# Performance work log

Measured on AMD Instinct MI355X. Metric: run time of the kernel, lower is better.

## Reference

```python
import jax, jax.numpy as jnp
import numpy as np
import math

D_MODEL = 1024
N_HEAD = 16
B, T = 4, 2048


def setup_inputs() -> dict:
    key = jax.random.key(0)
    ks = jax.random.split(key, 12)
    s = 1.0 / math.sqrt(D_MODEL)
    inp = {
        "q": jax.random.normal(ks[0], (B, T, D_MODEL), dtype=jnp.float32),
        "k": jax.random.normal(ks[1], (B, T, D_MODEL), dtype=jnp.float32),
        "v": jax.random.normal(ks[2], (B, T, D_MODEL), dtype=jnp.float32),
        "Wq": jax.random.uniform(ks[3], (D_MODEL, D_MODEL), jnp.float32, -s, s),
        "bq": jax.random.uniform(ks[4], (D_MODEL,), jnp.float32, -s, s),
        "Wk": jax.random.uniform(ks[5], (D_MODEL, D_MODEL), jnp.float32, -s, s),
        "bk": jax.random.uniform(ks[6], (D_MODEL,), jnp.float32, -s, s),
        "Wv": jax.random.uniform(ks[7], (D_MODEL, D_MODEL), jnp.float32, -s, s),
        "bv": jax.random.uniform(ks[8], (D_MODEL,), jnp.float32, -s, s),
        "Wo": jax.random.uniform(ks[9], (D_MODEL, D_MODEL), jnp.float32, -s, s),
        "bo": jax.random.uniform(ks[10], (D_MODEL,), jnp.float32, -s, s),
    }
    return inp


def reference(q, k, v, Wq, bq, Wk, bk, Wv, bv, Wo, bo):
    # NOTE: original module applies all three projections to `q` (k, v args unused)
    batch, time, dim = q.shape
    n_d = dim // N_HEAD
    # torch Linear: x @ W.T + b
    Q = (q @ Wq.T + bq).reshape(batch, time, N_HEAD, n_d).transpose(0, 2, 1, 3)
    K = (q @ Wk.T + bk).reshape(batch, time, N_HEAD, n_d).transpose(0, 2, 1, 3)
    V = (q @ Wv.T + bv).reshape(batch, time, N_HEAD, n_d).transpose(0, 2, 1, 3)
    # [B, H, T, T]
    score = jnp.einsum("bhqd,bhkd->bhqk", Q, K) / jnp.sqrt(jnp.float32(n_d))
    causal = jnp.tril(jnp.ones((time, time), dtype=bool))
    score = jnp.where(causal, score, -jnp.inf)
    # original uses Softmax(dim=-2): normalizes over the QUERY axis (faithful)
    attn = jax.nn.softmax(score, axis=-2)
    ctx = jnp.einsum("bhqk,bhkd->bhqd", attn, V)
    ctx = ctx.transpose(0, 2, 1, 3).reshape(batch, time, dim)
    return ctx @ Wo.T + bo
```

## Files before the change

### kernel.cpp

```cpp
#include <hip/hip_runtime.h>
#include <hip/hip_bf16.h>
#include <cstdint>
#include <cstddef>

typedef __bf16 bf16x8 __attribute__((ext_vector_type(8)));
typedef __bf16 bf16x4 __attribute__((ext_vector_type(4)));
typedef __bf16 bf16x2 __attribute__((ext_vector_type(2)));
typedef float  f32x4  __attribute__((ext_vector_type(4)));

static constexpr int TSEQ  = 2048;
static constexpr int DM    = 1024;
static constexpr int NH    = 16;
static constexpr int HD    = 64;
static constexpr int BATCH = 4;
static constexpr float SCL = 0.18033688011112042f;

__device__ __forceinline__ void gload16(const __bf16* g, __bf16* l) {
  __builtin_amdgcn_global_load_lds((const __attribute__((address_space(1))) void*)g,
                                   (__attribute__((address_space(3))) void*)l, 16, 0, 0);
}

#define PBAR()  asm volatile("s_barrier" ::: "memory")
#define LGKM()  asm volatile("s_waitcnt lgkmcnt(0)" ::: "memory")

__global__ __launch_bounds__(256) void cvt_kernel(const float* __restrict__ in,
                                                  __bf16* __restrict__ out, int n4) {
  int i = blockIdx.x * 256 + threadIdx.x;
  if (i < n4) {
    float4 v = reinterpret_cast<const float4*>(in)[i];
    bf16x4 o;
    o[0] = (__bf16)v.x; o[1] = (__bf16)v.y; o[2] = (__bf16)v.z; o[3] = (__bf16)v.w;
    reinterpret_cast<bf16x4*>(out)[i] = o;
  }
}

__global__ __launch_bounds__(256) void cvt4_kernel(
    const float* __restrict__ a, const float* __restrict__ bsrc,
    const float* __restrict__ c, const float* __restrict__ d,
    __bf16* __restrict__ oa, __bf16* __restrict__ ob,
    __bf16* __restrict__ oc, __bf16* __restrict__ od, int n4) {
  const float* src = (blockIdx.y == 0) ? a : (blockIdx.y == 1) ? bsrc
                    : (blockIdx.y == 2) ? c : d;
  __bf16* dst = (blockIdx.y == 0) ? oa : (blockIdx.y == 1) ? ob
               : (blockIdx.y == 2) ? oc : od;
  int i = blockIdx.x * 256 + threadIdx.x;
  if (i < n4) {
    float4 v = reinterpret_cast<const float4*>(src)[i];
    bf16x4 o;
    o[0] = (__bf16)v.x; o[1] = (__bf16)v.y; o[2] = (__bf16)v.z; o[3] = (__bf16)v.w;
    reinterpret_cast<bf16x4*>(dst)[i] = o;
  }
}

template <typename OUT_T>
__device__ __forceinline__ void gemm_body8(
    const __bf16* __restrict__ A, const __bf16* __restrict__ W,
    const float* __restrict__ bias, OUT_T* __restrict__ C,
    int i0, int o0, __bf16* lA, __bf16* lB) {
  const int tid = threadIdx.x;
  const int l = tid & 63, lr = l & 15, lg = l >> 4;
  const int w = tid >> 6;
  const int wr = w >> 2, wc = w & 3;

  f32x4 acc[8][4];
  const f32x4 fzero = {0.f, 0.f, 0.f, 0.f};
#pragma unroll
  for (int mi = 0; mi < 8; ++mi)
#pragma unroll
    for (int ni = 0; ni < 4; ++ni) acc[mi][ni] = fzero;

  const int s_row = tid >> 3;
  const int s_cc  = tid & 7;
  const __bf16* Ab = A + (size_t)i0 * DM;
  const __bf16* Wb = W + (size_t)o0 * DM;

  auto stage = [&](const __bf16* G, __bf16* L, int buf, int kt, int h) {
#pragma unroll
    for (int rr = 0; rr < 2; ++rr) {
      int row = h * 128 + rr * 64 + s_row;
      gload16(G + (size_t)row * DM + kt * 64 + ((s_cc ^ (row & 7)) << 3),
              L + buf * 16384 + (h * 128 + rr * 64) * 64 + tid * 8);
    }
  };
  auto rd = [&](const __bf16* base, int row, int ks) {
    int chunk = (ks * 4 + lg) ^ (row & 7);
    return *(const bf16x8*)(base + row * 64 + chunk * 8);
  };

  const int NT = DM / 64;

#pragma unroll
  for (int h = 0; h < 2; ++h) { stage(Ab, lA, 0, 0, h); stage(Wb, lB, 0, 0, h); }
#pragma unroll
  for (int h = 0; h < 2; ++h) { stage(Ab, lA, 1, 1, h); stage(Wb, lB, 1, 1, h); }
  asm volatile("s_waitcnt vmcnt(8)" ::: "memory");
  PBAR();

  for (int t = 0; t < NT; ++t) {
    const int cur = t & 1;
    const __bf16* cA = lA + cur * 16384;
    const __bf16* cB = lB + cur * 16384;
    const bool pre = (t + 2 < NT);

    bf16x8 afl[4][2], bfl[2][2], afh[4][2], bfh[2][2];

#pragma unroll
    for (int mi = 0; mi < 4; ++mi)
#pragma unroll
      for (int ks = 0; ks < 2; ++ks)
        afl[mi][ks] = rd(cA, wr * 64 + mi * 16 + lr, ks);
#pragma unroll
    for (int ni = 0; ni < 2; ++ni)
#pragma unroll
      for (int ks = 0; ks < 2; ++ks)
        bfl[ni][ks] = rd(cB, wc * 32 + ni * 16 + lr, ks);
    PBAR(); LGKM();
    __builtin_amdgcn_s_setprio(1);
#pragma unroll
    for (int mi = 0; mi < 4; ++mi)
#pragma unroll
      for (int ni = 0; ni < 2; ++ni)
#pragma unroll
        for (int ks = 0; ks < 2; ++ks)
          acc[mi][ni] = __builtin_amdgcn_mfma_f32_16x16x32_bf16(
              afl[mi][ks], bfl[ni][ks], acc[mi][ni], 0, 0, 0);
    __builtin_amdgcn_s_setprio(0);
    PBAR();

#pragma unroll
    for (int ni = 0; ni < 2; ++ni)
#pragma unroll
      for (int ks = 0; ks < 2; ++ks)
        bfh[ni][ks] = rd(cB, 128 + wc * 32 + ni * 16 + lr, ks);
    if (pre) stage(Wb, lB, cur, t + 2, 0);
    PBAR(); LGKM();
    __builtin_amdgcn_s_setprio(1);
#pragma unroll
    for (int mi = 0; mi < 4; ++mi)
#pragma unroll
      for (int ni = 0; ni < 2; ++ni)
#pragma unroll
        for (int ks = 0; ks < 2; ++ks)
          acc[mi][ni + 2] = __builtin_amdgcn_mfma_f32_16x16x32_bf16(
              afl[mi][ks], bfh[ni][ks], acc[mi][ni + 2], 0, 0, 0);
    __builtin_amdgcn_s_setprio(0);
    PBAR();

#pragma unroll
    for (int mi = 0; mi < 4; ++mi)
#pragma unroll
      for (int ks = 0; ks < 2; ++ks)
        afh[mi][ks] = rd(cA, 128 + wr * 64 + mi * 16 + lr, ks);
    if (pre) { stage(Ab, lA, cur, t + 2, 0); stage(Wb, lB, cur, t + 2, 1); }
    PBAR(); LGKM();
    __builtin_amdgcn_s_setprio(1);
#pragma unroll
    for (int mi = 0; mi < 4; ++mi)
#pragma unroll
      for (int ni = 0; ni < 2; ++ni)
#pragma unroll
        for (int ks = 0; ks < 2; ++ks)
          acc[mi + 4][ni] = __builtin_amdgcn_mfma_f32_16x16x32_bf16(
              afh[mi][ks], bfl[ni][ks], acc[mi + 4][ni], 0, 0, 0);
    __builtin_amdgcn_s_setprio(0);
    PBAR();

    if (pre) stage(Ab, lA, cur, t + 2, 1);
    if (pre)                asm volatile("s_waitcnt vmcnt(8)" ::: "memory");
    else if (t + 1 < NT)    asm volatile("s_waitcnt vmcnt(0)" ::: "memory");
    PBAR();
    __builtin_amdgcn_s_setprio(1);
#pragma unroll
    for (int mi = 0; mi < 4; ++mi)
#pragma unroll
      for (int ni = 0; ni < 2; ++ni)
#pragma unroll
        for (int ks = 0; ks < 2; ++ks)
          acc[mi + 4][ni + 2] = __builtin_amdgcn_mfma_f32_16x16x32_bf16(
              afh[mi][ks], bfh[ni][ks], acc[mi + 4][ni + 2], 0, 0, 0);
    __builtin_amdgcn_s_setprio(0);
    PBAR();
  }

#pragma unroll
  for (int ni = 0; ni < 4; ++ni) {
    int colb = (ni < 2) ? (wc * 32 + ni * 16) : (128 + wc * 32 + (ni - 2) * 16);
    int col = o0 + colb + lr;
    float bb = bias[col];
#pragma unroll
    for (int mi = 0; mi < 8; ++mi) {
      int rowb = (mi < 4) ? (wr * 64 + mi * 16) : (128 + wr * 64 + (mi - 4) * 16);
      int row = i0 + rowb + lg * 4;
#pragma unroll
      for (int r = 0; r < 4; ++r)
        C[(size_t)(row + r) * DM + col] = (OUT_T)(acc[mi][ni][r] + bb);
    }
  }
}

__global__ __launch_bounds__(512, 2) void gemm_qkv_kernel(
    const __bf16* __restrict__ A,
    const __bf16* __restrict__ W0, const __bf16* __restrict__ W1,
    const __bf16* __restrict__ W2,
    const float* __restrict__ b0, const float* __restrict__ b1,
    const float* __restrict__ b2,
    __bf16* __restrict__ O0, __bf16* __restrict__ O1, __bf16* __restrict__ O2) {
  __shared__ __align__(16) __bf16 lA[2 * 256 * 64];
  __shared__ __align__(16) __bf16 lB[2 * 256 * 64];
  const int flat = blockIdx.x;
  const int xcd = flat & 7, idx = flat >> 3;
  const int mi = xcd * 4 + idx / 12;
  const int nig = idx % 12;
  const int z = nig >> 2;
  const int o0 = (nig & 3) * 256;
  const __bf16* W = (z == 0) ? W0 : (z == 1) ? W1 : W2;
  const float* bias = (z == 0) ? b0 : (z == 1) ? b1 : b2;
  __bf16* C = (z == 0) ? O0 : (z == 1) ? O1 : O2;
  gemm_body8<__bf16>(A, W, bias, C, mi * 256, o0, lA, lB);
}

template <typename OUT_T>
__device__ __forceinline__ void gemm_body2(
    const __bf16* __restrict__ A, const __bf16* __restrict__ W,
    const float* __restrict__ bias, OUT_T* __restrict__ C,
    int i0, int o0, __bf16* lA, __bf16* lB) {
  const int tid = threadIdx.x;
  const int l = tid & 63, lr = l & 15, lg = l >> 4;
  const int w = tid >> 6;
  const int wr = w >> 2, wc = w & 3;

  f32x4 acc[4][4];
  const f32x4 fzero = {0.f, 0.f, 0.f, 0.f};
#pragma unroll
  for (int mi = 0; mi < 4; ++mi)
#pragma unroll
    for (int ni = 0; ni < 4; ++ni) acc[mi][ni] = fzero;

  const int s_row = tid >> 3;
  const int s_cc  = tid & 7;
  const int NT = DM / 64;

  {
#pragma unroll
    for (int n = 0; n < 2; ++n) {
      int row = n * 64 + s_row;
      gload16(A + (size_t)(i0 + row) * DM + ((s_cc ^ (row & 7)) << 3),
              lA + n * 4096 + tid * 8);
    }
#pragma unroll
    for (int n = 0; n < 4; ++n) {
      int row = n * 64 + s_row;
      gload16(W + (size_t)(o0 + row) * DM + ((s_cc ^ (row & 7)) << 3),
              lB + n * 4096 + tid * 8);
    }
  }
  asm volatile("s_waitcnt vmcnt(0)" ::: "memory");
  __syncthreads();

  for (int t = 0; t < NT; ++t) {
    const int cur = t & 1;
    if (t + 1 < NT) {
      const int k0 = (t + 1) * 64;
      const int nxt = cur ^ 1;
#pragma unroll
      for (int n = 0; n < 2; ++n) {
        int row = n * 64 + s_row;
        gload16(A + (size_t)(i0 + row) * DM + k0 + ((s_cc ^ (row & 7)) << 3),
                lA + nxt * 8192 + n * 4096 + tid * 8);
      }
#pragma unroll
      for (int n = 0; n < 4; ++n) {
        int row = n * 64 + s_row;
        gload16(W + (size_t)(o0 + row) * DM + k0 + ((s_cc ^ (row & 7)) << 3),
                lB + nxt * 16384 + n * 4096 + tid * 8);
      }
    }

    const __bf16* cA = lA + cur * 8192;
    const __bf16* cB = lB + cur * 16384;

    bf16x8 af[4][2], bf_[2][2];
#pragma unroll
    for (int mi = 0; mi < 4; ++mi)
#pragma unroll
      for (int ks = 0; ks < 2; ++ks) {
        int row = wr * 64 + mi * 16 + lr;
        int chunk = (ks * 4 + lg) ^ (row & 7);
        af[mi][ks] = *(const bf16x8*)(cA + row * 64 + chunk * 8);
      }
#pragma unroll
    for (int ni = 0; ni < 2; ++ni)
#pragma unroll
      for (int ks = 0; ks < 2; ++ks) {
        int row = wc * 64 + ni * 16 + lr;
        int chunk = (ks * 4 + lg) ^ (row & 7);
        bf_[ni][ks] = *(const bf16x8*)(cB + row * 64 + chunk * 8);
      }
    __builtin_amdgcn_s_setprio(1);
#pragma unroll
    for (int mi = 0; mi < 4; ++mi)
#pragma unroll
      for (int ni = 0; ni < 2; ++ni)
#pragma unroll
        for (int ks = 0; ks < 2; ++ks)
          acc[mi][ni] = __builtin_amdgcn_mfma_f32_16x16x32_bf16(
              af[mi][ks], bf_[ni][ks], acc[mi][ni], 0, 0, 0);
    __builtin_amdgcn_s_setprio(0);

#pragma unroll
    for (int ni = 0; ni < 2; ++ni)
#pragma unroll
      for (int ks = 0; ks < 2; ++ks) {
        int row = wc * 64 + (ni + 2) * 16 + lr;
        int chunk = (ks * 4 + lg) ^ (row & 7);
        bf_[ni][ks] = *(const bf16x8*)(cB + row * 64 + chunk * 8);
      }
    __builtin_amdgcn_s_setprio(1);
#pragma unroll
    for (int mi = 0; mi < 4; ++mi)
#pragma unroll
      for (int ni = 0; ni < 2; ++ni)
#pragma unroll
        for (int ks = 0; ks < 2; ++ks)
          acc[mi][ni + 2] = __builtin_amdgcn_mfma_f32_16x16x32_bf16(
              af[mi][ks], bf_[ni][ks], acc[mi][ni + 2], 0, 0, 0);
    __builtin_amdgcn_s_setprio(0);

    if (t + 1 < NT) {
      asm volatile("s_waitcnt vmcnt(0)" ::: "memory");
      __syncthreads();
    }
  }

#pragma unroll
  for (int ni = 0; ni < 4; ++ni) {
    int col = o0 + wc * 64 + ni * 16 + lr;
    float bb = bias[col];
#pragma unroll
    for (int mi = 0; mi < 4; ++mi) {
      int row = i0 + wr * 64 + mi * 16 + lg * 4;
#pragma unroll
      for (int r = 0; r < 4; ++r)
        C[(size_t)(row + r) * DM + col] = (OUT_T)(acc[mi][ni][r] + bb);
    }
  }
}

__global__ __launch_bounds__(512, 2) void gemm_out_kernel(
    const __bf16* __restrict__ A, const __bf16* __restrict__ W,
    const float* __restrict__ bias, float* __restrict__ C) {
  __shared__ __align__(16) __bf16 lA[2 * 128 * 64];
  __shared__ __align__(16) __bf16 lB[2 * 256 * 64];
  const int flat = blockIdx.x;
  const int xcd = flat & 7, idx = flat >> 3;
  const int mi = xcd * 8 + (idx & 7);
  const int ni = idx >> 3;
  gemm_body2<float>(A, W, bias, C, mi * 128, ni * 256, lA, lB);
}

__global__ __launch_bounds__(256) void colstats_kernel(
    const __bf16* __restrict__ Q, const __bf16* __restrict__ K,
    const __bf16* __restrict__ V, __bf16* __restrict__ VT) {
  const int flat = blockIdx.x;
  const int wid = (flat & 7) * 128 + (flat >> 3);
  const int g = wid >> 4, bx = wid & 15;
  const int h = g & 15, b = g >> 4;
  const int tid = threadIdx.x;
  const int w = tid >> 6, l = tid & 63, lr = l & 15, lg = l >> 4;
  const size_t base = (size_t)b * TSEQ * DM + (size_t)h * HD;

  __shared__ float part[4][64];
  __shared__ float invc[64];

  for (int ph = 0; ph < 2; ++ph) {
    const int kt = ph ? (31 - bx) : bx;
    const int k0 = kt * 64;

    bf16x8 kf[4][2];
#pragma unroll
    for (int ct = 0; ct < 4; ++ct)
#pragma unroll
      for (int ks = 0; ks < 2; ++ks)
        kf[ct][ks] = *(const bf16x8*)(K + base + (size_t)(k0 + ct * 16 + lr) * DM +
                                      ks * 32 + lg * 8);

    float csum[4] = {0.f, 0.f, 0.f, 0.f};
    const int nchunks = (TSEQ - k0) >> 4;
    for (int jj = w; jj < nchunks; jj += 4) {
      int qrow = k0 + jj * 16;
      bf16x8 a0 = *(const bf16x8*)(Q + base + (size_t)(qrow + lr) * DM + lg * 8);
      bf16x8 a1 = *(const bf16x8*)(Q + base + (size_t)(qrow + lr) * DM + 32 + lg * 8);
      const bool interior = (jj >= 4);
#pragma unroll
      for (int ct = 0; ct < 4; ++ct) {
        f32x4 s = {0.f, 0.f, 0.f, 0.f};
        s = __builtin_amdgcn_mfma_f32_16x16x32_bf16(a0, kf[ct][0], s, 0, 0, 0);
        s = __builtin_amdgcn_mfma_f32_16x16x32_bf16(a1, kf[ct][1], s, 0, 0, 0);
        if (interior) {
#pragma unroll
          for (int r = 0; r < 4; ++r) csum[ct] += __builtin_amdgcn_exp2f(s[r] * SCL);
        } else {
#pragma unroll
          for (int r = 0; r < 4; ++r) {
            int ql = jj * 16 + lg * 4 + r;
            int kl = ct * 16 + lr;
            float e = __builtin_amdgcn_exp2f(s[r] * SCL);
            csum[ct] += (ql >= kl) ? e : 0.f;
          }
        }
      }
    }

#pragma unroll
    for (int ct = 0; ct < 4; ++ct) {
      csum[ct] += __shfl_xor(csum[ct], 16, 64);
      csum[ct] += __shfl_xor(csum[ct], 32, 64);
    }

    if (l < 16) {
#pragma unroll
      for (int ct = 0; ct < 4; ++ct) part[w][ct * 16 + l] = csum[ct];
    }
    __syncthreads();
    if (tid < 64) {
      float c = part[0][tid] + part[1][tid] + part[2][tid] + part[3][tid];
      invc[tid] = 1.0f / c;
    }
    __syncthreads();

    const int d = tid >> 2, gq = tid & 3;
    size_t vtb = (((size_t)(b * NH + h)) * HD + d) * TSEQ + k0 + gq * 16;
#pragma unroll
    for (int kc = 0; kc < 16; kc += 2) {
      int kl = gq * 16 + kc;
      float v0 = (float)V[base + (size_t)(k0 + kl) * DM + d] * invc[kl];
      float v1 = (float)V[base + (size_t)(k0 + kl + 1) * DM + d] * invc[kl + 1];
      bf16x2 o; o[0] = (__bf16)v0; o[1] = (__bf16)v1;
      *(bf16x2*)(VT + vtb + kc) = o;
    }
    __syncthreads();
  }
}

__device__ __forceinline__ int swz(int e) { return e ^ (((e >> 6) & 7) << 3); }

__global__ __launch_bounds__(256, 4) void ctx_kernel(
    const __bf16* __restrict__ Q, const __bf16* __restrict__ K,
    const __bf16* __restrict__ VT, __bf16* __restrict__ CTX) {
  __shared__ __align__(16) __bf16 lK[4096];
  __shared__ __align__(16) __bf16 lV[4096];
  __shared__ __align__(16) __bf16 lP[8][16 * 88];
  const int flat = blockIdx.x;
  const int wid = (flat & 7) * 128 + (flat >> 3);
  const int g = wid >> 4, bx = wid & 15;
  const int h = g & 15, b = g >> 4;
  const int tid = threadIdx.x;
  const int w = tid >> 6, l = tid & 63, lr = l & 15, lg = l >> 4;
  const size_t base = (size_t)b * TSEQ * DM + (size_t)h * HD;
  const size_t vtb = ((size_t)(b * NH + h)) * HD * TSEQ;
  __bf16* pw1 = &lP[w][0];
  __bf16* pw2 = &lP[w + 4][0];

  const int qt1 = 31 - bx, qt2 = bx;
  const int q01 = qt1 * 64, q02 = qt2 * 64;

  const int srow = w * 8 + (l >> 3);
  const int scol = (((l & 7) ^ (l >> 3)) << 3);

  bf16x8 qf1[2], qf2[2];
#pragma unroll
  for (int ks = 0; ks < 2; ++ks) {
    qf1[ks] = *(const bf16x8*)(Q + base + (size_t)(q01 + w * 16 + lr) * DM + ks * 32 + lg * 8);
    qf2[ks] = *(const bf16x8*)(Q + base + (size_t)(q02 + w * 16 + lr) * DM + ks * 32 + lg * 8);
  }

  f32x4 acc1[4], acc2[4];
  const f32x4 fzero = {0.f, 0.f, 0.f, 0.f};
#pragma unroll
  for (int dt = 0; dt < 4; ++dt) { acc1[dt] = fzero; acc2[dt] = fzero; }

  for (int kt = 0; kt <= qt1; ++kt) {
    const int k0 = kt * 64;
    const bool two = (kt <= qt2);
    __syncthreads();
#pragma unroll
    for (int n = 0; n < 2; ++n) {
      gload16(K + base + (size_t)(k0 + n * 32 + srow) * DM + scol,
              lK + n * 2048 + w * 512);
      gload16(VT + vtb + (size_t)(n * 32 + srow) * TSEQ + k0 + scol,
              lV + n * 2048 + w * 512);
    }
    asm volatile("s_waitcnt vmcnt(0)" ::: "memory");
    __syncthreads();

    const bool diag1 = (kt == qt1), diag2 = (kt == qt2);
#pragma unroll
    for (int ct = 0; ct < 4; ++ct) {
      bf16x8 kb[2];
#pragma unroll
      for (int ks = 0; ks < 2; ++ks) {
        int e = (ct * 16 + lr) * 64 + ks * 32 + lg * 8;
        kb[ks] = *(const bf16x8*)(lK + swz(e));
      }
      {
        f32x4 s = {0.f, 0.f, 0.f, 0.f};
        s = __builtin_amdgcn_mfma_f32_16x16x32_bf16(kb[0], qf1[0], s, 0, 0, 0);
        s = __builtin_amdgcn_mfma_f32_16x16x32_bf16(kb[1], qf1[1], s, 0, 0, 0);
        bf16x4 pk;
        if (diag1) {
#pragma unroll
          for (int r = 0; r < 4; ++r) {
            int ql = w * 16 + lr, kl = ct * 16 + lg * 4 + r;
            pk[r] = (__bf16)((ql >= kl) ? __builtin_amdgcn_exp2f(s[r] * SCL) : 0.f);
          }
        } else {
#pragma unroll
          for (int r = 0; r < 4; ++r)
            pk[r] = (__bf16)__builtin_amdgcn_exp2f(s[r] * SCL);
        }
        *(bf16x4*)(pw1 + lr * 88 + ct * 16 + lg * 4) = pk;
      }
      if (two) {
        f32x4 s = {0.f, 0.f, 0.f, 0.f};
        s = __builtin_amdgcn_mfma_f32_16x16x32_bf16(kb[0], qf2[0], s, 0, 0, 0);
        s = __builtin_amdgcn_mfma_f32_16x16x32_bf16(kb[1], qf2[1], s, 0, 0, 0);
        bf16x4 pk;
        if (diag2) {
#pragma unroll
          for (int r = 0; r < 4; ++r) {
            int ql = w * 16 + lr, kl = ct * 16 + lg * 4 + r;
            pk[r] = (__bf16)((ql >= kl) ? __builtin_amdgcn_exp2f(s[r] * SCL) : 0.f);
          }
        } else {
#pragma unroll
          for (int r = 0; r < 4; ++r)
            pk[r] = (__bf16)__builtin_amdgcn_exp2f(s[r] * SCL);
        }
        *(bf16x4*)(pw2 + lr * 88 + ct * 16 + lg * 4) = pk;
      }
    }
    asm volatile("" ::: "memory");

    bf16x8 pa1[2], pa2[2];
#pragma unroll
    for (int ks = 0; ks < 2; ++ks)
      pa1[ks] = *(const bf16x8*)(pw1 + lr * 88 + ks * 32 + lg * 8);
    if (two) {
#pragma unroll
      for (int ks = 0; ks < 2; ++ks)
        pa2[ks] = *(const bf16x8*)(pw2 + lr * 88 + ks * 32 + lg * 8);
    }
#pragma unroll
    for (int dt = 0; dt < 4; ++dt) {
#pragma unroll
      for (int ks = 0; ks < 2; ++ks) {
        int e = (dt * 16 + lr) * 64 + ks * 32 + lg * 8;
        bf16x8 vb8 = *(const bf16x8*)(lV + swz(e));
        acc1[dt] = __builtin_amdgcn_mfma_f32_16x16x32_bf16(pa1[ks], vb8, acc1[dt], 0, 0, 0);
        if (two)
          acc2[dt] = __builtin_amdgcn_mfma_f32_16x16x32_bf16(pa2[ks], vb8, acc2[dt], 0, 0, 0);
      }
    }
  }

#pragma unroll
  for (int dt = 0; dt < 4; ++dt)
#pragma unroll
    for (int r = 0; r < 4; ++r) {
      CTX[base + (size_t)(q01 + w * 16 + lg * 4 + r) * DM + dt * 16 + lr] = (__bf16)acc1[dt][r];
      CTX[base + (size_t)(q02 + w * 16 + lg * 4 + r) * DM + dt * 16 + lr] = (__bf16)acc2[dt][r];
    }
}

extern "C" void kernel_launch(void* const* d_in, const int* in_sizes, int n_in,
                              void* d_out, int out_size, void* d_ws, size_t ws_size,
                              hipStream_t stream) {
  const float* q  = (const float*)d_in[0];
  const float* Wq = (const float*)d_in[3];
  const float* bq = (const float*)d_in[4];
  const float* Wk = (const float*)d_in[5];
  const float* bk = (const float*)d_in[6];
  const float* Wv = (const float*)d_in[7];
  const float* bv = (const float*)d_in[8];
  const float* Wo = (const float*)d_in[9];
  const float* bo = (const float*)d_in[10];
  float* out = (float*)d_out;

  const size_t NTOK = (size_t)BATCH * TSEQ;
  char* ws = (char*)d_ws;
  __bf16* qb  = (__bf16*)ws; ws += NTOK * DM * 2;
  __bf16* Wqb = (__bf16*)ws; ws += (size_t)DM * DM * 2;
  __bf16* Wkb = (__bf16*)ws; ws += (size_t)DM * DM * 2;
  __bf16* Wvb = (__bf16*)ws; ws += (size_t)DM * DM * 2;
  __bf16* Wob = (__bf16*)ws; ws += (size_t)DM * DM * 2;
  __bf16* Qp  = (__bf16*)ws; ws += NTOK * DM * 2;
  __bf16* Kp  = (__bf16*)ws; ws += NTOK * DM * 2;
  __bf16* Vp  = (__bf16*)ws; ws += NTOK * DM * 2;
  __bf16* VT  = (__bf16*)ws; ws += (size_t)BATCH * NH * HD * TSEQ * 2;
  __bf16* CTX = qb;

  const int nq4 = (int)(NTOK * DM / 4);
  const int nw4 = DM * DM / 4;
  cvt_kernel<<<(nq4 + 255) / 256, 256, 0, stream>>>(q, qb, nq4);
  cvt4_kernel<<<dim3((nw4 + 255) / 256, 4), 256, 0, stream>>>(
      Wq, Wk, Wv, Wo, Wqb, Wkb, Wvb, Wob, nw4);

  gemm_qkv_kernel<<<384, 512, 0, stream>>>(qb, Wqb, Wkb, Wvb, bq, bk, bv,
                                           Qp, Kp, Vp);

  colstats_kernel<<<1024, 256, 0, stream>>>(Qp, Kp, Vp, VT);
  ctx_kernel<<<1024, 256, 0, stream>>>(Qp, Kp, VT, CTX);

  gemm_out_kernel<<<256, 512, 0, stream>>>(CTX, Wob, bo, out);
}
```

Before: 208.7 us.

## Software-pipeline LDS fragment reads across GEMM phases and use contiguous warp tiles

The next tile's A-low and B-low fragments are now read from the other LDS buffer during the last MFMA phase of the current iteration. Partial lgkmcnt waits let the MFMAs start before every outstanding LDS read has returned. The warp-to-tile mapping changes from split halves (offset 128) to contiguous 128x64 per-warp blocks, and the epilogue indexing is updated to match. This is meant to hide LDS read latency behind matrix math. In exchange it keeps more fragment registers live across the loop and depends on correct ordering between the partial waits and the global-to-LDS staging.

Measured after the change: 234.3 us. 1.12x slower.

```diff
diff --git a/kernel.cpp b/kernel.cpp
--- a/kernel.cpp
+++ b/kernel.cpp
@@ -20,8 +20,8 @@
                                    (__attribute__((address_space(3))) void*)l, 16, 0, 0);
 }
 
-#define PBAR()  asm volatile("s_barrier" ::: "memory")
-#define LGKM()  asm volatile("s_waitcnt lgkmcnt(0)" ::: "memory")
+#define PBAR()   asm volatile("s_barrier" ::: "memory")
+#define LGKMN(n) asm volatile("s_waitcnt lgkmcnt(" #n ")" ::: "memory")
 
 __global__ __launch_bounds__(256) void cvt_kernel(const float* __restrict__ in,
                                                   __bf16* __restrict__ out, int n4) {
@@ -96,25 +96,33 @@
   asm volatile("s_waitcnt vmcnt(8)" ::: "memory");
   PBAR();
 
+  bf16x8 afl[4][2], afh[4][2], bfl[2][2], bfh[2][2];
+#pragma unroll
+  for (int mi = 0; mi < 4; ++mi)
+#pragma unroll
+    for (int ks = 0; ks < 2; ++ks)
+      afl[mi][ks] = rd(lA, wr * 128 + mi * 16 + lr, ks);
+#pragma unroll
+  for (int ni = 0; ni < 2; ++ni)
+#pragma unroll
+    for (int ks = 0; ks < 2; ++ks)
+      bfl[ni][ks] = rd(lB, wc * 64 + ni * 16 + lr, ks);
+
   for (int t = 0; t < NT; ++t) {
     const int cur = t & 1;
     const __bf16* cA = lA + cur * 16384;
     const __bf16* cB = lB + cur * 16384;
+    const __bf16* nA = lA + (cur ^ 1) * 16384;
+    const __bf16* nB = lB + (cur ^ 1) * 16384;
     const bool pre = (t + 2 < NT);
-
-    bf16x8 afl[4][2], bfl[2][2], afh[4][2], bfh[2][2];
-
-#pragma unroll
-    for (int mi = 0; mi < 4; ++mi)
+    const bool hasnext = (t + 1 < NT);
+
+#pragma unroll
+    for (int ni = 0; ni < 2; ++ni)
 #pragma unroll
       for (int ks = 0; ks < 2; ++ks)
-        afl[mi][ks] = rd(cA, wr * 64 + mi * 16 + lr, ks);
-#pragma unroll
-    for (int ni = 0; ni < 2; ++ni)
-#pragma unroll
-      for (int ks = 0; ks < 2; ++ks)
-        bfl[ni][ks] = rd(cB, wc * 32 + ni * 16 + lr, ks);
-    PBAR(); LGKM();
+        bfh[ni][ks] = rd(cB, wc * 64 + (ni + 2) * 16 + lr, ks);
+    PBAR(); LGKMN(4);
     __builtin_amdgcn_s_setprio(1);
 #pragma unroll
     for (int mi = 0; mi < 4; ++mi)
@@ -128,12 +136,12 @@
     PBAR();
 
 #pragma unroll
-    for (int ni = 0; ni < 2; ++ni)
+    for (int mi = 0; mi < 4; ++mi)
 #pragma unroll
       for (int ks = 0; ks < 2; ++ks)
-        bfh[ni][ks] = rd(cB, 128 + wc * 32 + ni * 16 + lr, ks);
+        afh[mi][ks] = rd(cA, wr * 128 + (mi + 4) * 16 + lr, ks);
     if (pre) stage(Wb, lB, cur, t + 2, 0);
-    PBAR(); LGKM();
+    PBAR(); LGKMN(8);
     __builtin_amdgcn_s_setprio(1);
 #pragma unroll
     for (int mi = 0; mi < 4; ++mi)
@@ -146,13 +154,8 @@
     __builtin_amdgcn_s_setprio(0);
     PBAR();
 
-#pragma unroll
-    for (int mi = 0; mi < 4; ++mi)
-#pragma unroll
-      for (int ks = 0; ks < 2; ++ks)
-        afh[mi][ks] = rd(cA, 128 + wr * 64 + mi * 16 + lr, ks);
-    if (pre) { stage(Ab, lA, cur, t + 2, 0); stage(Wb, lB, cur, t + 2, 1); }
-    PBAR(); LGKM();
+    if (pre) { stage(Wb, lB, cur, t + 2, 1); stage(Ab, lA, cur, t + 2, 0); }
+    PBAR(); LGKMN(0);
     __builtin_amdgcn_s_setprio(1);
 #pragma unroll
     for (int mi = 0; mi < 4; ++mi)
@@ -166,9 +169,21 @@
     PBAR();
 
     if (pre) stage(Ab, lA, cur, t + 2, 1);
-    if (pre)                asm volatile("s_waitcnt vmcnt(8)" ::: "memory");
-    else if (t + 1 < NT)    asm volatile("s_waitcnt vmcnt(0)" ::: "memory");
+    if (pre)             asm volatile("s_waitcnt vmcnt(8)" ::: "memory");
+    else if (hasnext)    asm volatile("s_waitcnt vmcnt(0)" ::: "memory");
     PBAR();
+    if (hasnext) {
+#pragma unroll
+      for (int mi = 0; mi < 4; ++mi)
+#pragma unroll
+        for (int ks = 0; ks < 2; ++ks)
+          afl[mi][ks] = rd(nA, wr * 128 + mi * 16 + lr, ks);
+#pragma unroll
+      for (int ni = 0; ni < 2; ++ni)
+#pragma unroll
+        for (int ks = 0; ks < 2; ++ks)
+          bfl[ni][ks] = rd(nB, wc * 64 + ni * 16 + lr, ks);
+    }
     __builtin_amdgcn_s_setprio(1);
 #pragma unroll
     for (int mi = 0; mi < 4; ++mi)
@@ -184,13 +199,11 @@
 
 #pragma unroll
   for (int ni = 0; ni < 4; ++ni) {
-    int colb = (ni < 2) ? (wc * 32 + ni * 16) : (128 + wc * 32 + (ni - 2) * 16);
-    int col = o0 + colb + lr;
+    int col = o0 + wc * 64 + ni * 16 + lr;
     float bb = bias[col];
 #pragma unroll
     for (int mi = 0; mi < 8; ++mi) {
-      int rowb = (mi < 4) ? (wr * 64 + mi * 16) : (128 + wr * 64 + (mi - 4) * 16);
-      int row = i0 + rowb + lg * 4;
+      int row = i0 + wr * 128 + mi * 16 + lg * 4;
 #pragma unroll
       for (int r = 0; r < 4; ++r)
         C[(size_t)(row + r) * DM + col] = (OUT_T)(acc[mi][ni][r] + bb);
```

## Retile fused QKV GEMM to 256x192 tiles over concatenated weights

Applied to the files above, without the earlier changes.

The three projection weights are stored contiguously so the QKV GEMM can treat them as one 8192x3072 problem. It is retiled from 256x256 tiles (384 blocks) to 256x192 tiles (512 blocks), with each warp covering 128 rows by 48 columns and the B staging split into three 64-row chunks. The goal is to fill all 256 CUs evenly with two blocks each and to cut the LDS footprint. The trade-off is less operand reuse per tile, plus the epilogue now picks the bias and output buffer per column.

New measurement: 209.1 us. About the same (+0.2%).

```diff
diff --git a/kernel.cpp b/kernel.cpp
--- a/kernel.cpp
+++ b/kernel.cpp
@@ -52,37 +52,49 @@
   }
 }
 
-template <typename OUT_T>
-__device__ __forceinline__ void gemm_body8(
-    const __bf16* __restrict__ A, const __bf16* __restrict__ W,
-    const float* __restrict__ bias, OUT_T* __restrict__ C,
-    int i0, int o0, __bf16* lA, __bf16* lB) {
+__global__ __launch_bounds__(512, 2) void gemm_qkv_kernel(
+    const __bf16* __restrict__ A, const __bf16* __restrict__ Wqkv,
+    const float* __restrict__ b0, const float* __restrict__ b1,
+    const float* __restrict__ b2, __bf16* __restrict__ QKVp) {
+  __shared__ __align__(16) __bf16 lA[2 * 256 * 64];
+  __shared__ __align__(16) __bf16 lB[2 * 192 * 64];
+  const int flat = blockIdx.x;
+  const int xcd = flat & 7, idx = flat >> 3;
+  const int mi = xcd * 4 + (idx & 3);
+  const int nig = idx >> 2;
+  const int i0 = mi * 256, o0 = nig * 192;
+
   const int tid = threadIdx.x;
   const int l = tid & 63, lr = l & 15, lg = l >> 4;
   const int w = tid >> 6;
   const int wr = w >> 2, wc = w & 3;
 
-  f32x4 acc[8][4];
+  f32x4 acc[8][3];
   const f32x4 fzero = {0.f, 0.f, 0.f, 0.f};
 #pragma unroll
-  for (int mi = 0; mi < 8; ++mi)
-#pragma unroll
-    for (int ni = 0; ni < 4; ++ni) acc[mi][ni] = fzero;
+  for (int mm = 0; mm < 8; ++mm)
+#pragma unroll
+    for (int ni = 0; ni < 3; ++ni) acc[mm][ni] = fzero;
 
   const int s_row = tid >> 3;
   const int s_cc  = tid & 7;
   const __bf16* Ab = A + (size_t)i0 * DM;
-  const __bf16* Wb = W + (size_t)o0 * DM;
-
-  auto stage = [&](const __bf16* G, __bf16* L, int buf, int kt, int h) {
+  const __bf16* Wb = Wqkv + (size_t)o0 * DM;
+
+  auto stageA = [&](int buf, int kt, int h) {
 #pragma unroll
     for (int rr = 0; rr < 2; ++rr) {
       int row = h * 128 + rr * 64 + s_row;
-      gload16(G + (size_t)row * DM + kt * 64 + ((s_cc ^ (row & 7)) << 3),
-              L + buf * 16384 + (h * 128 + rr * 64) * 64 + tid * 8);
+      gload16(Ab + (size_t)row * DM + kt * 64 + ((s_cc ^ (row & 7)) << 3),
+              lA + buf * 16384 + (h * 128 + rr * 64) * 64 + tid * 8);
     }
   };
-  auto rd = [&](const __bf16* base, int row, int ks) {
+  auto stageB = [&](int buf, int kt, int n) {
+    int row = n * 64 + s_row;
+    gload16(Wb + (size_t)row * DM + kt * 64 + ((s_cc ^ (row & 7)) << 3),
+            lB + buf * 12288 + n * 4096 + tid * 8);
+  };
+  auto rdA = [&](const __bf16* base, int row, int ks) {
     int chunk = (ks * 4 + lg) ^ (row & 7);
     return *(const bf16x8*)(base + row * 64 + chunk * 8);
   };
@@ -90,133 +102,111 @@
   const int NT = DM / 64;
 
 #pragma unroll
-  for (int h = 0; h < 2; ++h) { stage(Ab, lA, 0, 0, h); stage(Wb, lB, 0, 0, h); }
-#pragma unroll
-  for (int h = 0; h < 2; ++h) { stage(Ab, lA, 1, 1, h); stage(Wb, lB, 1, 1, h); }
-  asm volatile("s_waitcnt vmcnt(8)" ::: "memory");
+  for (int h = 0; h < 2; ++h) stageA(0, 0, h);
+#pragma unroll
+  for (int n = 0; n < 3; ++n) stageB(0, 0, n);
+#pragma unroll
+  for (int h = 0; h < 2; ++h) stageA(1, 1, h);
+#pragma unroll
+  for (int n = 0; n < 3; ++n) stageB(1, 1, n);
+  asm volatile("s_waitcnt vmcnt(7)" ::: "memory");
   PBAR();
 
   for (int t = 0; t < NT; ++t) {
     const int cur = t & 1;
     const __bf16* cA = lA + cur * 16384;
-    const __bf16* cB = lB + cur * 16384;
+    const __bf16* cB = lB + cur * 12288;
     const bool pre = (t + 2 < NT);
 
-    bf16x8 afl[4][2], bfl[2][2], afh[4][2], bfh[2][2];
-
-#pragma unroll
-    for (int mi = 0; mi < 4; ++mi)
+    bf16x8 afl[4][2], afh[4][2], bfl[2][2], bfh[1][2];
+
+#pragma unroll
+    for (int mm = 0; mm < 4; ++mm)
 #pragma unroll
       for (int ks = 0; ks < 2; ++ks)
-        afl[mi][ks] = rd(cA, wr * 64 + mi * 16 + lr, ks);
+        afl[mm][ks] = rdA(cA, wr * 128 + mm * 16 + lr, ks);
 #pragma unroll
     for (int ni = 0; ni < 2; ++ni)
 #pragma unroll
       for (int ks = 0; ks < 2; ++ks)
-        bfl[ni][ks] = rd(cB, wc * 32 + ni * 16 + lr, ks);
+        bfl[ni][ks] = rdA(cB, wc * 48 + ni * 16 + lr, ks);
     PBAR(); LGKM();
     __builtin_amdgcn_s_setprio(1);
 #pragma unroll
-    for (int mi = 0; mi < 4; ++mi)
+    for (int mm = 0; mm < 4; ++mm)
 #pragma unroll
       for (int ni = 0; ni < 2; ++ni)
 #pragma unroll
         for (int ks = 0; ks < 2; ++ks)
-          acc[mi][ni] = __builtin_amdgcn_mfma_f32_16x16x32_bf16(
-              afl[mi][ks], bfl[ni][ks], acc[mi][ni], 0, 0, 0);
+          acc[mm][ni] = __builtin_amdgcn_mfma_f32_16x16x32_bf16(
+              afl[mm][ks], bfl[ni][ks], acc[mm][ni], 0, 0, 0);
     __builtin_amdgcn_s_setprio(0);
     PBAR();
 
 #pragma unroll
-    for (int ni = 0; ni < 2; ++ni)
-#pragma unroll
-      for (int ks = 0; ks < 2; ++ks)
-        bfh[ni][ks] = rd(cB, 128 + wc * 32 + ni * 16 + lr, ks);
-    if (pre) stage(Wb, lB, cur, t + 2, 0);
+    for (int ks = 0; ks < 2; ++ks)
+      bfh[0][ks] = rdA(cB, wc * 48 + 2 * 16 + lr, ks);
+    if (pre) { stageB(cur, t + 2, 0); stageB(cur, t + 2, 1); }
     PBAR(); LGKM();
     __builtin_amdgcn_s_setprio(1);
 #pragma unroll
-    for (int mi = 0; mi < 4; ++mi)
-#pragma unroll
-      for (int ni = 0; ni < 2; ++ni)
-#pragma unroll
-        for (int ks = 0; ks < 2; ++ks)
-          acc[mi][ni + 2] = __builtin_amdgcn_mfma_f32_16x16x32_bf16(
-              afl[mi][ks], bfh[ni][ks], acc[mi][ni + 2], 0, 0, 0);
+    for (int mm = 0; mm < 4; ++mm)
+#pragma unroll
+      for (int ks = 0; ks < 2; ++ks)
+        acc[mm][2] = __builtin_amdgcn_mfma_f32_16x16x32_bf16(
+            afl[mm][ks], bfh[0][ks], acc[mm][2], 0, 0, 0);
     __builtin_amdgcn_s_setprio(0);
     PBAR();
 
 #pragma unroll
-    for (int mi = 0; mi < 4; ++mi)
+    for (int mm = 0; mm < 4; ++mm)
 #pragma unroll
       for (int ks = 0; ks < 2; ++ks)
-        afh[mi][ks] = rd(cA, 128 + wr * 64 + mi * 16 + lr, ks);
-    if (pre) { stage(Ab, lA, cur, t + 2, 0); stage(Wb, lB, cur, t + 2, 1); }
+        afh[mm][ks] = rdA(cA, wr * 128 + (mm + 4) * 16 + lr, ks);
+    if (pre) { stageB(cur, t + 2, 2); stageA(cur, t + 2, 0); }
     PBAR(); LGKM();
     __builtin_amdgcn_s_setprio(1);
 #pragma unroll
-    for (int mi = 0; mi < 4; ++mi)
+    for (int mm = 0; mm < 4; ++mm)
 #pragma unroll
       for (int ni = 0; ni < 2; ++ni)
 #pragma unroll
         for (int ks = 0; ks < 2; ++ks)
-          acc[mi + 4][ni] = __builtin_amdgcn_mfma_f32_16x16x32_bf16(
-              afh[mi][ks], bfl[ni][ks], acc[mi + 4][ni], 0, 0, 0);
+          acc[mm + 4][ni] = __builtin_amdgcn_mfma_f32_16x16x32_bf16(
+              afh[mm][ks], bfl[ni][ks], acc[mm + 4][ni], 0, 0, 0);
     __builtin_amdgcn_s_setprio(0);
     PBAR();
 
-    if (pre) stage(Ab, lA, cur, t + 2, 1);
-    if (pre)                asm volatile("s_waitcnt vmcnt(8)" ::: "memory");
+    if (pre) stageA(cur, t + 2, 1);
+    if (pre)                asm volatile("s_waitcnt vmcnt(7)" ::: "memory");
     else if (t + 1 < NT)    asm volatile("s_waitcnt vmcnt(0)" ::: "memory");
     PBAR();
     __builtin_amdgcn_s_setprio(1);
 #pragma unroll
-    for (int mi = 0; mi < 4; ++mi)
-#pragma unroll
-      for (int ni = 0; ni < 2; ++ni)
-#pragma unroll
-        for (int ks = 0; ks < 2; ++ks)
-          acc[mi + 4][ni + 2] = __builtin_amdgcn_mfma_f32_16x16x32_bf16(
-              afh[mi][ks], bfh[ni][ks], acc[mi + 4][ni + 2], 0, 0, 0);
+    for (int mm = 0; mm < 4; ++mm)
+#pragma unroll
+      for (int ks = 0; ks < 2; ++ks)
+        acc[mm + 4][2] = __builtin_amdgcn_mfma_f32_16x16x32_bf16(
+            afh[mm][ks], bfh[0][ks], acc[mm + 4][2], 0, 0, 0);
     __builtin_amdgcn_s_setprio(0);
     PBAR();
   }
 
 #pragma unroll
-  for (int ni = 0; ni < 4; ++ni) {
-    int colb = (ni < 2) ? (wc * 32 + ni * 16) : (128 + wc * 32 + (ni - 2) * 16);
-    int col = o0 + colb + lr;
-    float bb = bias[col];
-#pragma unroll
-    for (int mi = 0; mi < 8; ++mi) {
-      int rowb = (mi < 4) ? (wr * 64 + mi * 16) : (128 + wr * 64 + (mi - 4) * 16);
-      int row = i0 + rowb + lg * 4;
+  for (int ni = 0; ni < 3; ++ni) {
+    int col = o0 + wc * 48 + ni * 16 + lr;
+    int z = col >> 10, cin = col & 1023;
+    const float* bp = (z == 0) ? b0 : (z == 1) ? b1 : b2;
+    float bb = bp[cin];
+    __bf16* O = QKVp + (size_t)z * 8192 * DM;
+#pragma unroll
+    for (int mm = 0; mm < 8; ++mm) {
+      int row = i0 + wr * 128 + mm * 16 + lg * 4;
 #pragma unroll
       for (int r = 0; r < 4; ++r)
-        C[(size_t)(row + r) * DM + col] = (OUT_T)(acc[mi][ni][r] + bb);
-    }
-  }
-}
-
-__global__ __launch_bounds__(512, 2) void gemm_qkv_kernel(
-    const __bf16* __restrict__ A,
-    const __bf16* __restrict__ W0, const __bf16* __restrict__ W1,
-    const __bf16* __restrict__ W2,
-    const float* __restrict__ b0, const float* __restrict__ b1,
-    const float* __restrict__ b2,
-    __bf16* __restrict__ O0, __bf16* __restrict__ O1, __bf16* __restrict__ O2) {
-  __shared__ __align__(16) __bf16 lA[2 * 256 * 64];
-  __shared__ __align__(16) __bf16 lB[2 * 256 * 64];
-  const int flat = blockIdx.x;
-  const int xcd = flat & 7, idx = flat >> 3;
-  const int mi = xcd * 4 + idx / 12;
-  const int nig = idx % 12;
-  const int z = nig >> 2;
-  const int o0 = (nig & 3) * 256;
-  const __bf16* W = (z == 0) ? W0 : (z == 1) ? W1 : W2;
-  const float* bias = (z == 0) ? b0 : (z == 1) ? b1 : b2;
-  __bf16* C = (z == 0) ? O0 : (z == 1) ? O1 : O2;
-  gemm_body8<__bf16>(A, W, bias, C, mi * 256, o0, lA, lB);
+        O[(size_t)(row + r) * DM + cin] = (__bf16)(acc[mm][ni][r] + bb);
+    }
+  }
 }
 
 template <typename OUT_T>
@@ -588,25 +578,24 @@
 
   const size_t NTOK = (size_t)BATCH * TSEQ;
   char* ws = (char*)d_ws;
-  __bf16* qb  = (__bf16*)ws; ws += NTOK * DM * 2;
-  __bf16* Wqb = (__bf16*)ws; ws += (size_t)DM * DM * 2;
-  __bf16* Wkb = (__bf16*)ws; ws += (size_t)DM * DM * 2;
-  __bf16* Wvb = (__bf16*)ws; ws += (size_t)DM * DM * 2;
-  __bf16* Wob = (__bf16*)ws; ws += (size_t)DM * DM * 2;
-  __bf16* Qp  = (__bf16*)ws; ws += NTOK * DM * 2;
-  __bf16* Kp  = (__bf16*)ws; ws += NTOK * DM * 2;
-  __bf16* Vp  = (__bf16*)ws; ws += NTOK * DM * 2;
-  __bf16* VT  = (__bf16*)ws; ws += (size_t)BATCH * NH * HD * TSEQ * 2;
+  __bf16* qb   = (__bf16*)ws; ws += NTOK * DM * 2;
+  __bf16* Wqkv = (__bf16*)ws; ws += 3 * (size_t)DM * DM * 2;
+  __bf16* Wob  = (__bf16*)ws; ws += (size_t)DM * DM * 2;
+  __bf16* QKVp = (__bf16*)ws; ws += 3 * NTOK * DM * 2;
+  __bf16* VT   = (__bf16*)ws; ws += (size_t)BATCH * NH * HD * TSEQ * 2;
   __bf16* CTX = qb;
+
+  __bf16* Qp = QKVp;
+  __bf16* Kp = QKVp + NTOK * DM;
+  __bf16* Vp = QKVp + 2 * NTOK * DM;
 
   const int nq4 = (int)(NTOK * DM / 4);
   const int nw4 = DM * DM / 4;
   cvt_kernel<<<(nq4 + 255) / 256, 256, 0, stream>>>(q, qb, nq4);
   cvt4_kernel<<<dim3((nw4 + 255) / 256, 4), 256, 0, stream>>>(
-      Wq, Wk, Wv, Wo, Wqb, Wkb, Wvb, Wob, nw4);
-
-  gemm_qkv_kernel<<<384, 512, 0, stream>>>(qb, Wqb, Wkb, Wvb, bq, bk, bv,
-                                           Qp, Kp, Vp);
+      Wq, Wk, Wv, Wo, Wqkv, Wqkv + (size_t)DM * DM, Wqkv + 2 * (size_t)DM * DM, Wob, nw4);
+
+  gemm_qkv_kernel<<<512, 512, 0, stream>>>(qb, Wqkv, bq, bk, bv, QKVp);
 
   colstats_kernel<<<1024, 256, 0, stream>>>(Qp, Kp, Vp, VT);
   ctx_kernel<<<1024, 256, 0, stream>>>(Qp, Kp, VT, CTX);
```
